# Kernel optimization log

Hardware: AMD Instinct MI355X
Metric: run time of the kernel (lower is better)

Reference implementation:

```python
import jax, jax.numpy as jnp
import numpy as np

B, IN, H = 8192, 1024, 1024


def setup_inputs() -> dict:
    key = jax.random.key(0)
    ks = jax.random.split(key, 12)
    s_in = 1.0 / np.sqrt(IN + H)  # torch Linear default init scale
    inp = {
        "x": jax.random.normal(ks[0], (B, IN), jnp.float32),
        "h_prev": jax.random.normal(ks[1], (B, H), jnp.float32),
        "c_prev": jax.random.normal(ks[2], (B, H), jnp.float32),
        "embed": jax.random.normal(ks[3], (B, H), jnp.float32),
    }
    for i, g in enumerate(("forget", "input", "update", "out")):
        inp[f"W_{g}"] = jax.random.uniform(ks[4 + 2 * i], (IN + H, H), jnp.float32, -s_in, s_in)
        inp[f"b_{g}"] = jax.random.uniform(ks[5 + 2 * i], (H,), jnp.float32, -s_in, s_in)
    return inp


def reference(x, h_prev, c_prev, embed,
              W_forget, b_forget, W_input, b_input,
              W_update, b_update, W_out, b_out):
    # cat_input: [B, IN+H]; embed is accepted but unused (matches source forward)
    cat_input = jnp.concatenate((x.reshape(x.shape[0], -1), h_prev), axis=1)
    # Fuse the 4 gate GEMMs into one [B, IN+H] x [IN+H, 4H] matmul (same math)
    W = jnp.concatenate((W_forget, W_input, W_update, W_out), axis=1)  # [IN+H, 4H]
    b = jnp.concatenate((b_forget, b_input, b_update, b_out))          # [4H]
    gates = cat_input @ W + b                                          # [B, 4H]
    f_t, i_t, g_t, o_t = jnp.split(gates, 4, axis=1)
    f_t = jax.nn.sigmoid(f_t)
    i_t = jax.nn.sigmoid(i_t)
    c_opt = jnp.tanh(g_t)
    c_t = c_prev * f_t + i_t * c_opt
    o_t = jax.nn.sigmoid(o_t)
    h_t = o_t * jnp.tanh(c_t)
    return (h_t, c_t)
```

## Files before the change

kernel.cpp:

```cpp
#include <hip/hip_runtime.h>
#include <hip/hip_bf16.h>


typedef __attribute__((ext_vector_type(8))) short short8;
typedef __attribute__((ext_vector_type(4))) float f32x4;

#define GLOBAL_AS __attribute__((address_space(1)))
#define LDS_AS    __attribute__((address_space(3)))

__device__ __forceinline__ void load_lds16(const void* g, void* l) {
  __builtin_amdgcn_global_load_lds((const GLOBAL_AS unsigned int*)g,
                                   (LDS_AS unsigned int*)l, 16, 0, 0);
}

__device__ __forceinline__ unsigned short f2bf(float f) {
  unsigned int u = __float_as_uint(f);
  return (unsigned short)((u + 0x7FFFu + ((u >> 16) & 1u)) >> 16);
}
__device__ __forceinline__ float sigf(float x) { return 1.0f / (1.0f + __expf(-x)); }
__device__ __forceinline__ float tanh_fast(float x) {
  return 1.0f - 2.0f / (__expf(2.0f * x) + 1.0f);
}

__global__ void pack_kernel(const float* __restrict__ x,
                            const float* __restrict__ h,
                            const float* __restrict__ W0,
                            const float* __restrict__ W1,
                            const float* __restrict__ W2,
                            const float* __restrict__ W3,
                            unsigned short* __restrict__ Apk,
                            unsigned short* __restrict__ Wp) {
  int blk = blockIdx.x;
  if (blk < 8192) {
    int t = blk * 256 + threadIdx.x;
    int row = t >> 8;
    int c   = t & 255;
    int k   = c << 3;
    const float* src = (k < 1024) ? (x + (size_t)row * 1024 + k)
                                  : (h + (size_t)row * 1024 + (k - 1024));
    float4 f0 = ((const float4*)src)[0];
    float4 f1 = ((const float4*)src)[1];
    union { unsigned short us[8]; uint4 v; } u;
    u.us[0] = f2bf(f0.x); u.us[1] = f2bf(f0.y);
    u.us[2] = f2bf(f0.z); u.us[3] = f2bf(f0.w);
    u.us[4] = f2bf(f1.x); u.us[5] = f2bf(f1.y);
    u.us[6] = f2bf(f1.z); u.us[7] = f2bf(f1.w);
    *(uint4*)(Apk + (size_t)row * 2048 + c * 8) = u.v;
  } else {
    int b  = blk - 8192;
    int c  = b & 255;
    int nb = (b >> 8) & 3;
    int g  = b >> 10;
    const float* Wg = (g == 0) ? W0 : (g == 1) ? W1 : (g == 2) ? W2 : W3;
    int np = nb * 256 + threadIdx.x;
    int kbase = c << 3;
    union { unsigned short us[8]; uint4 v; } u;
#pragma unroll
    for (int j = 0; j < 8; ++j)
      u.us[j] = f2bf(Wg[(size_t)(kbase + j) * 1024 + np]);
    int n = (g << 10) + np;
    *(uint4*)(Wp + (size_t)n * 2048 + c * 8) = u.v;
  }
}

#define MFMA16(va, vb, vc) __builtin_amdgcn_mfma_f32_16x16x32_bf16(va, vb, vc, 0, 0, 0)

#define PH(ARd, rdRing, mQ, DOB, BRd, ACm, BCm, QOFF, stSlot, stIsA, DOVM)     \
  {                                                                            \
    const int rr_ = (rdRing);                                                  \
    _Pragma("unroll")                                                          \
    for (int mm = 0; mm < 4; ++mm)                                             \
      ARd[mm] = *(const short8*)&LDSu[rr_ * 8192 + aRdBase + ((mQ) * 4 + mm) * 512]; \
    if (DOB) {                                                                 \
      _Pragma("unroll")                                                        \
      for (int gg = 0; gg < 4; ++gg)                                           \
        BRd[gg] = *(const short8*)&LDSu[32768 + rr_ * 8192 + bRdBase + gg * 512]; \
    }                                                                          \
    {                                                                          \
      int ss_ = (stSlot); ss_ = ss_ > 63 ? 63 : ss_;                           \
      const int so_ = ss_ * 32;                                                \
      const int pb_ = ((stSlot) & 3) * 8192;                                   \
      if (stIsA) {                                                             \
        load_lds16(aSrc0 + so_, &LDSu[pb_ + wv * 512]);                        \
        load_lds16(aSrc1 + so_, &LDSu[pb_ + 4096 + wv * 512]);                 \
      } else {                                                                 \
        load_lds16(bSrc0 + so_, &LDSu[32768 + pb_ + wv * 512]);                \
        load_lds16(bSrc1 + so_, &LDSu[32768 + pb_ + 4096 + wv * 512]);         \
      }                                                                        \
    }                                                                          \
    __builtin_amdgcn_s_barrier();                                              \
    __builtin_amdgcn_s_setprio(1);                                             \
    _Pragma("unroll")                                                          \
    for (int mm = 0; mm < 4; ++mm) {                                           \
      _Pragma("unroll")                                                        \
      for (int gg = 0; gg < 4; ++gg)                                           \
        acc[(QOFF) + mm][gg] = MFMA16(ACm[mm], BCm[gg], acc[(QOFF) + mm][gg]); \
    }                                                                          \
    __builtin_amdgcn_s_setprio(0);                                             \
    if (DOVM) asm volatile("s_waitcnt vmcnt(6)");                              \
    __builtin_amdgcn_s_barrier();                                              \
  }

__global__ __launch_bounds__(512, 2) void lstm_gemm_kernel(
    const unsigned short* __restrict__ Apk,
    const unsigned short* __restrict__ Wp,
    const float* __restrict__ c_prev,
    const float* __restrict__ bF, const float* __restrict__ bI,
    const float* __restrict__ bU, const float* __restrict__ bO,
    float* __restrict__ outH, float* __restrict__ outC) {
  extern __shared__ unsigned short LDSu[];

  const int tid = threadIdx.x;
  const int l   = tid & 63;
  const int wv  = tid >> 6;
  const int wr  = wv >> 2;
  const int wc  = wv & 3;

  int bid = blockIdx.x;
  int wg  = ((bid & 7) << 6) | (bid >> 3);
  const int mblk = wg >> 4;
  const int nblk = wg & 15;
  const int brow = mblk << 8;

  const int rl  = l & 15;
  const int cg  = l >> 4;
  const int sc  = cg ^ ((rl >> 1) & 3);
  const int aRdBase = (wr * 128 + rl) * 32 + sc * 8;
  const int bRdBase = (wc * 64 + rl) * 32 + sc * 8;

  const int srow = wv * 16 + (l >> 2);
  const int csw  = ((l & 3) ^ ((l >> 3) & 3)) * 8;
  const unsigned short* aSrc0 = Apk + (size_t)(brow + srow) * 2048 + csw;
  const unsigned short* aSrc1 = aSrc0 + (size_t)128 * 2048;
  int p0 = nblk * 256 + srow;
  int n0 = (((p0 >> 4) & 3) << 10) | ((p0 >> 6) << 4) | (p0 & 15);
  int p1 = p0 + 128;
  int n1 = (((p1 >> 4) & 3) << 10) | ((p1 >> 6) << 4) | (p1 & 15);
  const unsigned short* bSrc0 = Wp + (size_t)n0 * 2048 + csw;
  const unsigned short* bSrc1 = Wp + (size_t)n1 * 2048 + csw;

  f32x4 acc[8][4];
#pragma unroll
  for (int m = 0; m < 8; ++m)
#pragma unroll
    for (int g = 0; g < 4; ++g) acc[m][g] = (f32x4)0.0f;

  load_lds16(aSrc0 + 0,  &LDSu[0 + wv * 512]);
  load_lds16(aSrc1 + 0,  &LDSu[4096 + wv * 512]);
  load_lds16(bSrc0 + 0,  &LDSu[32768 + wv * 512]);
  load_lds16(bSrc1 + 0,  &LDSu[32768 + 4096 + wv * 512]);
  load_lds16(aSrc0 + 32, &LDSu[8192 + wv * 512]);
  load_lds16(aSrc1 + 32, &LDSu[8192 + 4096 + wv * 512]);
  load_lds16(bSrc0 + 32, &LDSu[32768 + 8192 + wv * 512]);
  load_lds16(bSrc1 + 32, &LDSu[32768 + 8192 + 4096 + wv * 512]);
  load_lds16(aSrc0 + 64, &LDSu[16384 + wv * 512]);
  load_lds16(aSrc1 + 64, &LDSu[16384 + 4096 + wv * 512]);
  load_lds16(bSrc0 + 64, &LDSu[32768 + 16384 + wv * 512]);
  load_lds16(bSrc1 + 64, &LDSu[32768 + 16384 + 4096 + wv * 512]);
  asm volatile("s_waitcnt vmcnt(8)");
  __builtin_amdgcn_s_barrier();

  short8 a0[4], a1[4], b0[4], b1[4];
#pragma unroll
  for (int mm = 0; mm < 4; ++mm)
    a0[mm] = *(const short8*)&LDSu[aRdBase + mm * 512];
#pragma unroll
  for (int gg = 0; gg < 4; ++gg)
    b0[gg] = *(const short8*)&LDSu[32768 + bRdBase + gg * 512];

#pragma unroll 1
  for (int u = 0; u < 32; ++u) {
    const int ra = (u & 1) << 1;
    const int rb = ra | 1;
    const int rc = 2 - ra;
    const int s3 = 2 * u + 3;
    const int s4 = 2 * u + 4;
    PH(a1, ra, 1, 0, b1, a0, b0, 0, s3, 1, 1)
    PH(a0, rb, 0, 1, b1, a1, b0, 4, s3, 0, 0)
    PH(a1, rb, 1, 0, b0, a0, b1, 0, s4, 1, 1)
    PH(a0, rc, 0, 1, b0, a1, b1, 4, s4, 0, 0)
  }

  const int colh = nblk * 64 + wc * 16 + rl;
  const float biasF = bF[colh], biasI = bI[colh];
  const float biasU = bU[colh], biasO = bO[colh];
  const int row0 = brow + wr * 128 + ((l >> 4) << 2);
#pragma unroll
  for (int m = 0; m < 8; ++m) {
#pragma unroll
    for (int r = 0; r < 4; ++r) {
      int row = row0 + m * 16 + r;
      size_t idx = (size_t)row * 1024 + colh;
      float f  = sigf(acc[m][0][r] + biasF);
      float i_ = sigf(acc[m][1][r] + biasI);
      float g_ = tanh_fast(acc[m][2][r] + biasU);
      float o_ = sigf(acc[m][3][r] + biasO);
      float cp = c_prev[idx];
      float cn = cp * f + i_ * g_;
      outH[idx] = o_ * tanh_fast(cn);
      outC[idx] = cn;
    }
  }
}

extern "C" void kernel_launch(void* const* d_in, const int* in_sizes, int n_in,
                              void* d_out, int out_size, void* d_ws, size_t ws_size,
                              hipStream_t stream) {
  const float* x      = (const float*)d_in[0];
  const float* h_prev = (const float*)d_in[1];
  const float* c_prev = (const float*)d_in[2];
  const float* Wf = (const float*)d_in[4];
  const float* bf = (const float*)d_in[5];
  const float* Wi = (const float*)d_in[6];
  const float* bi = (const float*)d_in[7];
  const float* Wu = (const float*)d_in[8];
  const float* bu = (const float*)d_in[9];
  const float* Wo = (const float*)d_in[10];
  const float* bo = (const float*)d_in[11];

  unsigned short* Apk = (unsigned short*)d_ws;
  unsigned short* Wp  = (unsigned short*)((char*)d_ws + (size_t)8192 * 2048 * 2);

  pack_kernel<<<12288, 256, 0, stream>>>(x, h_prev, Wf, Wi, Wu, Wo, Apk, Wp);

  hipFuncSetAttribute((const void*)lstm_gemm_kernel,
                      hipFuncAttributeMaxDynamicSharedMemorySize, 131072);

  float* outH = (float*)d_out;
  float* outC = outH + (size_t)8192 * 1024;
  lstm_gemm_kernel<<<512, 512, 131072, stream>>>(Apk, Wp, c_prev,
                                                 bf, bi, bu, bo, outH, outC);
}
```

Before: 183.5 us.

## Replace interleaved ping-pong MFMA pipeline with simple per-stage LDS-ring loop

Removes the four-phase macro schedule, which split A/B fragment reads across half-tiles, double-buffered register fragments and used two barriers per phase. The main loop now handles one K-stage per iteration: it issues global-to-LDS prefetches three stages ahead into a 4-slot ring, reads all 8 A and 4 B fragments, runs 32 MFMAs, then does a single vmcnt wait and one barrier. This cuts barrier count and simplifies the code. In exchange, LDS read latency is no longer overlapped with the previous phase's MFMAs within a wave, so overlap now depends on other waves and the second resident block.

```diff
diff --git a/kernel.cpp b/kernel.cpp
--- a/kernel.cpp
+++ b/kernel.cpp
@@ -65,42 +65,6 @@
 
 #define MFMA16(va, vb, vc) __builtin_amdgcn_mfma_f32_16x16x32_bf16(va, vb, vc, 0, 0, 0)
 
-#define PH(ARd, rdRing, mQ, DOB, BRd, ACm, BCm, QOFF, stSlot, stIsA, DOVM)     \
-  {                                                                            \
-    const int rr_ = (rdRing);                                                  \
-    _Pragma("unroll")                                                          \
-    for (int mm = 0; mm < 4; ++mm)                                             \
-      ARd[mm] = *(const short8*)&LDSu[rr_ * 8192 + aRdBase + ((mQ) * 4 + mm) * 512]; \
-    if (DOB) {                                                                 \
-      _Pragma("unroll")                                                        \
-      for (int gg = 0; gg < 4; ++gg)                                           \
-        BRd[gg] = *(const short8*)&LDSu[32768 + rr_ * 8192 + bRdBase + gg * 512]; \
-    }                                                                          \
-    {                                                                          \
-      int ss_ = (stSlot); ss_ = ss_ > 63 ? 63 : ss_;                           \
-      const int so_ = ss_ * 32;                                                \
-      const int pb_ = ((stSlot) & 3) * 8192;                                   \
-      if (stIsA) {                                                             \
-        load_lds16(aSrc0 + so_, &LDSu[pb_ + wv * 512]);                        \
-        load_lds16(aSrc1 + so_, &LDSu[pb_ + 4096 + wv * 512]);                 \
-      } else {                                                                 \
-        load_lds16(bSrc0 + so_, &LDSu[32768 + pb_ + wv * 512]);                \
-        load_lds16(bSrc1 + so_, &LDSu[32768 + pb_ + 4096 + wv * 512]);         \
-      }                                                                        \
-    }                                                                          \
-    __builtin_amdgcn_s_barrier();                                              \
-    __builtin_amdgcn_s_setprio(1);                                             \
-    _Pragma("unroll")                                                          \
-    for (int mm = 0; mm < 4; ++mm) {                                           \
-      _Pragma("unroll")                                                        \
-      for (int gg = 0; gg < 4; ++gg)                                           \
-        acc[(QOFF) + mm][gg] = MFMA16(ACm[mm], BCm[gg], acc[(QOFF) + mm][gg]); \
-    }                                                                          \
-    __builtin_amdgcn_s_setprio(0);                                             \
-    if (DOVM) asm volatile("s_waitcnt vmcnt(6)");                              \
-    __builtin_amdgcn_s_barrier();                                              \
-  }
-
 __global__ __launch_bounds__(512, 2) void lstm_gemm_kernel(
     const unsigned short* __restrict__ Apk,
     const unsigned short* __restrict__ Wp,
@@ -145,40 +109,47 @@
 #pragma unroll
     for (int g = 0; g < 4; ++g) acc[m][g] = (f32x4)0.0f;
 
-  load_lds16(aSrc0 + 0,  &LDSu[0 + wv * 512]);
-  load_lds16(aSrc1 + 0,  &LDSu[4096 + wv * 512]);
-  load_lds16(bSrc0 + 0,  &LDSu[32768 + wv * 512]);
-  load_lds16(bSrc1 + 0,  &LDSu[32768 + 4096 + wv * 512]);
-  load_lds16(aSrc0 + 32, &LDSu[8192 + wv * 512]);
-  load_lds16(aSrc1 + 32, &LDSu[8192 + 4096 + wv * 512]);
-  load_lds16(bSrc0 + 32, &LDSu[32768 + 8192 + wv * 512]);
-  load_lds16(bSrc1 + 32, &LDSu[32768 + 8192 + 4096 + wv * 512]);
-  load_lds16(aSrc0 + 64, &LDSu[16384 + wv * 512]);
-  load_lds16(aSrc1 + 64, &LDSu[16384 + 4096 + wv * 512]);
-  load_lds16(bSrc0 + 64, &LDSu[32768 + 16384 + wv * 512]);
-  load_lds16(bSrc1 + 64, &LDSu[32768 + 16384 + 4096 + wv * 512]);
+#pragma unroll
+  for (int s = 0; s < 3; ++s) {
+    const int pb = s * 8192;
+    const int so = s * 32;
+    load_lds16(aSrc0 + so, &LDSu[pb + wv * 512]);
+    load_lds16(aSrc1 + so, &LDSu[pb + 4096 + wv * 512]);
+    load_lds16(bSrc0 + so, &LDSu[32768 + pb + wv * 512]);
+    load_lds16(bSrc1 + so, &LDSu[32768 + pb + 4096 + wv * 512]);
+  }
   asm volatile("s_waitcnt vmcnt(8)");
   __builtin_amdgcn_s_barrier();
 
-  short8 a0[4], a1[4], b0[4], b1[4];
-#pragma unroll
-  for (int mm = 0; mm < 4; ++mm)
-    a0[mm] = *(const short8*)&LDSu[aRdBase + mm * 512];
-#pragma unroll
-  for (int gg = 0; gg < 4; ++gg)
-    b0[gg] = *(const short8*)&LDSu[32768 + bRdBase + gg * 512];
-
 #pragma unroll 1
-  for (int u = 0; u < 32; ++u) {
-    const int ra = (u & 1) << 1;
-    const int rb = ra | 1;
-    const int rc = 2 - ra;
-    const int s3 = 2 * u + 3;
-    const int s4 = 2 * u + 4;
-    PH(a1, ra, 1, 0, b1, a0, b0, 0, s3, 1, 1)
-    PH(a0, rb, 0, 1, b1, a1, b0, 4, s3, 0, 0)
-    PH(a1, rb, 1, 0, b0, a0, b1, 0, s4, 1, 1)
-    PH(a0, rc, 0, 1, b0, a1, b1, 4, s4, 0, 0)
+  for (int s = 0; s < 64; ++s) {
+    const int ring  = (s & 3) * 8192;
+    const int pring = ((s + 3) & 3) * 8192;
+    int sp = s + 3; sp = sp > 63 ? 63 : sp;
+    const int so = sp * 32;
+    load_lds16(aSrc0 + so, &LDSu[pring + wv * 512]);
+    load_lds16(aSrc1 + so, &LDSu[pring + 4096 + wv * 512]);
+    load_lds16(bSrc0 + so, &LDSu[32768 + pring + wv * 512]);
+    load_lds16(bSrc1 + so, &LDSu[32768 + pring + 4096 + wv * 512]);
+
+    short8 bfr[4], afr[8];
+#pragma unroll
+    for (int g = 0; g < 4; ++g)
+      bfr[g] = *(const short8*)&LDSu[32768 + ring + bRdBase + g * 512];
+#pragma unroll
+    for (int m = 0; m < 8; ++m)
+      afr[m] = *(const short8*)&LDSu[ring + aRdBase + m * 512];
+
+    __builtin_amdgcn_s_setprio(1);
+#pragma unroll
+    for (int m = 0; m < 8; ++m)
+#pragma unroll
+      for (int g = 0; g < 4; ++g)
+        acc[m][g] = MFMA16(afr[m], bfr[g], acc[m][g]);
+    __builtin_amdgcn_s_setprio(0);
+
+    asm volatile("s_waitcnt vmcnt(8)");
+    __builtin_amdgcn_s_barrier();
   }
 
   const int colh = nblk * 64 + wc * 16 + rl;
```

After: 183.9 us. No clear change (+0.2%).
